# Kernel tuning notes

Measured on AMD Instinct MI355X. Metric: run time of the kernel, lower is better.

The kernel has to match this reference:

```python
import jax, jax.numpy as jnp
import numpy as np
from jax import lax

B, C, H, W = 8, 512, 64, 64
HM, WM = 256, 256
EPS = 1e-08


def _nearest_downsample(mask, H_out, W_out):
    # torch F.interpolate(mode='nearest'): src_idx = floor(dst_idx * in/out)
    h_in, w_in = mask.shape[-2:]
    ri = (jnp.arange(H_out) * h_in) // H_out
    ci = (jnp.arange(W_out) * w_in) // W_out
    return mask[:, :, ri][:, :, :, ci]


def _dilate3x3(m):
    # binary dilation with 3x3 ones structuring element == 3x3 max-pool, zero pad
    return lax.reduce_window(m, 0.0, lax.max, (1, 1, 3, 3), (1, 1, 1, 1),
                             [(0, 0), (0, 0), (1, 1), (1, 1)])


def _edt(mask2d):
    # Exact Euclidean distance from each pixel to nearest mask==1 pixel.
    # mask2d: [B, H, W] float 0/1. Separable two-pass squared EDT.
    b, h, w = mask2d.shape
    BIG = jnp.asarray(h + w, mask2d.dtype)
    rows = jnp.arange(h)
    di = jnp.abs(rows[:, None] - rows[None, :]).astype(mask2d.dtype)  # [H, H']
    # g[b,i,j] = min_{i'} |i - i'| s.t. mask[b,i',j]==1 (BIG if column empty)
    g = jnp.min(di[None, :, :, None] + BIG * (1.0 - mask2d)[:, None, :, :], axis=2)  # [B,H,W]
    cols = jnp.arange(w)
    dj2 = ((cols[:, None] - cols[None, :]) ** 2).astype(mask2d.dtype)  # [W, W']
    d2 = jnp.min(g[:, :, None, :] ** 2 + dj2[None, None, :, :], axis=3)  # [B,H,W]
    dist = jnp.sqrt(d2)
    dist = dist / (jnp.max(dist, axis=(1, 2), keepdims=True) + 1e-06)
    return dist


def setup_inputs() -> dict:
    key = jax.random.key(0)
    k1, k2, k3, k4, k5 = jax.random.split(key, 5)
    f_s = jax.random.normal(k1, (B, C, H, W), dtype=jnp.float32)
    support_mask = jax.random.randint(k2, (B, 1, HM, WM), 0, 2, dtype=jnp.int32)
    sg = 1.0 / np.sqrt(C)
    gate_w = jax.random.uniform(k3, (C, C), jnp.float32, -sg, sg)
    gate_b = jnp.zeros((C,), jnp.float32)
    sf = 1.0 / np.sqrt(C + 1)
    fusion_w = jax.random.uniform(k4, (C, C + 1), jnp.float32, -sf, sf)
    fusion_b = jnp.zeros((C,), jnp.float32)
    return {"f_s": f_s, "support_mask": support_mask, "gate_w": gate_w,
            "gate_b": gate_b, "fusion_w": fusion_w, "fusion_b": fusion_b}


def reference(f_s, support_mask, gate_w, gate_b, fusion_w, fusion_b):
    m_s = _nearest_downsample(support_mask, f_s.shape[2], f_s.shape[3]).astype(f_s.dtype)  # [B,1,H,W]
    m_dil = _dilate3x3(m_s)
    m_bg = jnp.clip(m_dil - m_s, 0.0, None)

    p_fg = jnp.sum(f_s * m_s, axis=(2, 3)) / (jnp.sum(m_s, axis=(2, 3)) + EPS)   # [B,C]
    p_bg = jnp.sum(f_s * m_bg, axis=(2, 3)) / (jnp.sum(m_bg, axis=(2, 3)) + EPS)  # [B,C]
    p_contrast = (p_fg - p_bg)[:, :, None, None]

    gate = jax.nn.sigmoid(jnp.einsum('bchw,oc->bohw', f_s, gate_w) + gate_b[None, :, None, None])
    f_pur = f_s + gate * p_contrast

    dist = _edt(m_s[:, 0])[:, None]  # [B,1,H,W]
    x = jnp.concatenate([f_pur, dist], axis=1)  # [B,C+1,H,W]
    out = jnp.einsum('bchw,oc->bohw', x, fusion_w) + fusion_b[None, :, None, None]
    return jax.nn.relu(out)
```

## Files before the change

kernel.cpp:

```cpp
#include <hip/hip_runtime.h>
#include <math.h>

#define NB 8
#define CC 512
#define NPIX 4096
#define HM 256

#define WS_MS    0
#define WS_MBG   32768
#define WS_DIST  65536
#define WS_CNT   98304
#define WS_PC    98320
#define WS_GWP   102416
#define WS_FWP   364560
#define WS_FSPK  626704
#define WS_FPPK  17403920

typedef __attribute__((ext_vector_type(8))) short short8;
typedef __attribute__((ext_vector_type(4))) float f32x4;

__device__ __forceinline__ uint32_t packbf(float x) {
    uint32_t b = __float_as_uint(x);
    uint32_t hi = (b + 0x7fffu + ((b >> 16) & 1u)) & 0xffff0000u;
    float rem = x - __uint_as_float(hi);
    uint32_t rb = __float_as_uint(rem);
    uint32_t lo = (rb + 0x7fffu + ((rb >> 16) & 1u)) >> 16;
    return hi | lo;
}
__device__ __forceinline__ float unpackf(uint32_t u) {
    return __uint_as_float(u & 0xffff0000u) + __uint_as_float(u << 16);
}

__device__ __forceinline__ float wave_sum(float v) {
#pragma unroll
    for (int o = 32; o > 0; o >>= 1) v += __shfl_down(v, o, 64);
    return v;
}
__device__ __forceinline__ float wave_max(float v) {
#pragma unroll
    for (int o = 32; o > 0; o >>= 1) v = fmaxf(v, __shfl_down(v, o, 64));
    return v;
}

__global__ __launch_bounds__(1024) void mask_edt_kernel(
    const int* __restrict__ mask, float* __restrict__ ms, float* __restrict__ mbg,
    float* __restrict__ dist, float* __restrict__ cnt)
{
    __shared__ float sm[4096];
    __shared__ float sg[4096];
    __shared__ float red[32];

    const int b = blockIdx.x;
    const int t = threadIdx.x;
    const int wid = t >> 6, lane = t & 63;
    const int* mb = mask + b * (HM * HM);

#pragma unroll
    for (int u = 0; u < 4; ++u) {
        int p = u * 1024 + t;
        int i = p >> 6, j = p & 63;
        sm[p] = (float)mb[(i * 4) * HM + (j * 4)];
    }
    __syncthreads();

    float cfg = 0.f, cbg = 0.f;
#pragma unroll
    for (int u = 0; u < 4; ++u) {
        int p = u * 1024 + t;
        int i = p >> 6, j = p & 63;
        float mx = 0.f;
#pragma unroll
        for (int di = -1; di <= 1; ++di) {
            int ii = i + di;
            if (ii < 0 || ii > 63) continue;
#pragma unroll
            for (int dj = -1; dj <= 1; ++dj) {
                int jj = j + dj;
                if (jj < 0 || jj > 63) continue;
                mx = fmaxf(mx, sm[ii * 64 + jj]);
            }
        }
        float m = sm[p];
        float bg = fmaxf(mx - m, 0.f);
        cfg += m; cbg += bg;
        ms[b * NPIX + p] = m;
        mbg[b * NPIX + p] = bg;
    }
    float s1 = wave_sum(cfg), s2 = wave_sum(cbg);
    if (lane == 0) { red[wid] = s1; red[16 + wid] = s2; }
    __syncthreads();
    if (t == 0) {
        float a = 0.f, g = 0.f;
#pragma unroll
        for (int w = 0; w < 16; ++w) { a += red[w]; g += red[16 + w]; }
        cnt[b] = a; cnt[8 + b] = g;
    }

#pragma unroll 1
    for (int u = 0; u < 4; ++u) {
        int p = u * 1024 + t;
        int i = p >> 6, j = p & 63;
        float fi = (float)i;
        float best = 1e30f;
#pragma unroll 8
        for (int ii = 0; ii < 64; ++ii) {
            float v = fabsf(fi - (float)ii) + 128.f * (1.f - sm[ii * 64 + j]);
            best = fminf(best, v);
        }
        sg[p] = best;
    }
    __syncthreads();

    float dmx = 0.f;
#pragma unroll 1
    for (int u = 0; u < 4; ++u) {
        int p = u * 1024 + t;
        int i = p >> 6, j = p & 63;
        float fj = (float)j;
        float best = 1e30f;
#pragma unroll 8
        for (int jj = 0; jj < 64; ++jj) {
            float g = sg[i * 64 + jj];
            float dj = fj - (float)jj;
            best = fminf(best, fmaf(g, g, dj * dj));
        }
        float d = sqrtf(best);
        sm[p] = d;
        dmx = fmaxf(dmx, d);
    }
    __syncthreads();
    float mW = wave_max(dmx);
    if (lane == 0) red[wid] = mW;
    __syncthreads();
    float dmax = red[0];
#pragma unroll
    for (int w = 1; w < 16; ++w) dmax = fmaxf(dmax, red[w]);
    dmax += 1e-6f;
#pragma unroll
    for (int u = 0; u < 4; ++u) {
        int p = u * 1024 + t;
        dist[b * NPIX + p] = sm[p] / dmax;
    }
}

__global__ __launch_bounds__(256) void pcontrast_kernel(
    const float* __restrict__ F, const float* __restrict__ ms,
    const float* __restrict__ mbg, const float* __restrict__ cnt,
    float* __restrict__ pc)
{
    const int c = blockIdx.x, b = blockIdx.y, t = threadIdx.x;
    const float4* f4 = (const float4*)(F + ((size_t)b * CC + c) * NPIX);
    const float4* m4 = (const float4*)(ms + (size_t)b * NPIX);
    const float4* g4 = (const float4*)(mbg + (size_t)b * NPIX);
    float sfg = 0.f, sbg = 0.f;
#pragma unroll 4
    for (int idx = t; idx < NPIX / 4; idx += 256) {
        float4 v = f4[idx], m = m4[idx], g = g4[idx];
        sfg += v.x * m.x + v.y * m.y + v.z * m.z + v.w * m.w;
        sbg += v.x * g.x + v.y * g.y + v.z * g.z + v.w * g.w;
    }
    __shared__ float r1[4], r2[4];
    sfg = wave_sum(sfg); sbg = wave_sum(sbg);
    int wid = t >> 6, lane = t & 63;
    if (lane == 0) { r1[wid] = sfg; r2[wid] = sbg; }
    __syncthreads();
    if (t == 0) {
        float a = r1[0] + r1[1] + r1[2] + r1[3];
        float g = r2[0] + r2[1] + r2[2] + r2[3];
        pc[b * CC + c] = a / (cnt[b] + 1e-8f) - g / (cnt[8 + b] + 1e-8f);
    }
}

__global__ __launch_bounds__(256) void transpose_pack(
    const float* __restrict__ F, uint32_t* __restrict__ Fp)
{
    __shared__ float sm[64][65];
    const int b  = blockIdx.z;
    const int c0 = blockIdx.y * 64;
    const int p0 = blockIdx.x * 64;
    const int t  = threadIdx.x;
    const float* Fb = F + ((size_t)b * CC + c0) * NPIX + p0;
#pragma unroll
    for (int s = 0; s < 4; ++s) {
        int cl = s * 16 + (t >> 4);
        float4 v = *(const float4*)&Fb[(size_t)cl * NPIX + (t & 15) * 4];
        *(float4*)&sm[cl][(t & 15) * 4] = v;
    }
    __syncthreads();
    const int lane = t & 63, w = t >> 6;
    uint32_t* Op = Fp + ((size_t)b * NPIX + p0) * CC + c0;
#pragma unroll
    for (int s = 0; s < 16; ++s) {
        int pl = s * 4 + w;
        Op[(size_t)pl * CC + lane] = packbf(sm[lane][pl]);
    }
}

__global__ __launch_bounds__(256) void pack_weights(
    const float* __restrict__ gw, const float* __restrict__ fw,
    uint32_t* __restrict__ gwp, uint32_t* __restrict__ fwp)
{
    const int o = blockIdx.x, t = threadIdx.x;
#pragma unroll 2
    for (int c = t; c < CC; c += 256) {
        gwp[o * CC + c] = packbf(gw[o * CC + c]);
        fwp[o * CC + c] = packbf(fw[o * (CC + 1) + c]);
    }
}

template <int MODE>
__global__ __launch_bounds__(256, 4) void mfma_gemm(
    const uint32_t* __restrict__ Apk, const uint32_t* __restrict__ Bpk,
    long aStride, long bStride,
    const float* __restrict__ bias,
    const float* __restrict__ aux,
    const float* __restrict__ wsrc,
    void* __restrict__ outp)
{
    const int gx = gridDim.x, gy = gridDim.y;
    const int nwg = gx * gy * gridDim.z;
    int lin = (blockIdx.z * gy + blockIdx.y) * gx + blockIdx.x;
    int cpx = nwg >> 3;
    int swz = (lin & 7) * cpx + (lin >> 3);
    const int bx = swz % gx;
    const int by = (swz / gx) % gy;
    const int b  = swz / (gx * gy);

    const int nBase = bx * 128;
    const int mBase = by * 128;
    const int tid   = threadIdx.x;
    const int lane  = tid & 63, wid = tid >> 6;
    const int wr    = wid >> 1, wc = wid & 1;

    __shared__ uint32_t As[128 * 32];
    __shared__ uint32_t Bs[128 * 32];

    const uint32_t* Ab = Apk + (size_t)b * aStride;
    const uint32_t* Bb = Bpk + (size_t)b * bStride;

    f32x4 acc[4][4];
#pragma unroll
    for (int i = 0; i < 4; ++i)
#pragma unroll
        for (int j = 0; j < 4; ++j) acc[i][j] = (f32x4){0.f, 0.f, 0.f, 0.f};

    const int l8 = lane >> 3;
    const int k16src = (lane & 7) ^ l8;
    const int fr = lane & 15;
    const int kc = lane >> 4;

    for (int it = 0; it < 16; ++it) {
        const int ktU = it * 32;
#pragma unroll
        for (int r = 0; r < 4; ++r) {
            int grp = r * 4 + wid;
            int row = grp * 8 + l8;
            const uint32_t* gA = Ab + (size_t)(mBase + row) * CC + ktU + k16src * 4;
            const uint32_t* gB = Bb + (size_t)(nBase + row) * CC + ktU + k16src * 4;
            __builtin_amdgcn_global_load_lds(
                (const __attribute__((address_space(1))) uint32_t*)gA,
                (__attribute__((address_space(3))) uint32_t*)&As[grp * 256 + lane * 4], 16, 0, 0);
            __builtin_amdgcn_global_load_lds(
                (const __attribute__((address_space(1))) uint32_t*)gB,
                (__attribute__((address_space(3))) uint32_t*)&Bs[grp * 256 + lane * 4], 16, 0, 0);
        }
        __syncthreads();

        short8 hA[4], lA[4];
#pragma unroll
        for (int fm = 0; fm < 4; ++fm) {
            int row = wr * 64 + fm * 16 + fr;
            int base = row * 32, s = row & 7;
            uint4 x0 = *(const uint4*)&As[base + (((kc * 2)     ^ s) << 2)];
            uint4 x1 = *(const uint4*)&As[base + (((kc * 2 + 1) ^ s) << 2)];
            uint32_t pk[8] = {x0.x, x0.y, x0.z, x0.w, x1.x, x1.y, x1.z, x1.w};
#pragma unroll
            for (int j = 0; j < 8; ++j) {
                hA[fm][j] = (short)(pk[j] >> 16);
                lA[fm][j] = (short)(pk[j] & 0xffffu);
            }
        }
#pragma unroll
        for (int fn = 0; fn < 4; ++fn) {
            int row = wc * 64 + fn * 16 + fr;
            int base = row * 32, s = row & 7;
            uint4 x0 = *(const uint4*)&Bs[base + (((kc * 2)     ^ s) << 2)];
            uint4 x1 = *(const uint4*)&Bs[base + (((kc * 2 + 1) ^ s) << 2)];
            uint32_t pk[8] = {x0.x, x0.y, x0.z, x0.w, x1.x, x1.y, x1.z, x1.w};
            short8 hB, lB;
#pragma unroll
            for (int j = 0; j < 8; ++j) {
                hB[j] = (short)(pk[j] >> 16);
                lB[j] = (short)(pk[j] & 0xffffu);
            }
#pragma unroll
            for (int fm = 0; fm < 4; ++fm) {
                acc[fm][fn] = __builtin_amdgcn_mfma_f32_16x16x32_bf16(hA[fm], hB, acc[fm][fn], 0, 0, 0);
                acc[fm][fn] = __builtin_amdgcn_mfma_f32_16x16x32_bf16(hA[fm], lB, acc[fm][fn], 0, 0, 0);
                acc[fm][fn] = __builtin_amdgcn_mfma_f32_16x16x32_bf16(lA[fm], hB, acc[fm][fn], 0, 0, 0);
            }
        }
        __syncthreads();
    }

    const int rrow = (lane >> 4) * 4;
    if constexpr (MODE == 0) {
        uint32_t* fpur = (uint32_t*)outp;
#pragma unroll
        for (int fn = 0; fn < 4; ++fn) {
            int o = nBase + wc * 64 + fn * 16 + fr;
            float bo  = bias[o];
            float pco = aux[(size_t)b * CC + o];
#pragma unroll
            for (int fm = 0; fm < 4; ++fm) {
#pragma unroll
                for (int r = 0; r < 4; ++r) {
                    int p = mBase + wr * 64 + fm * 16 + rrow + r;
                    size_t idx = (size_t)p * CC + o;
                    float fs = unpackf(Ab[idx]);
                    float z = acc[fm][fn][r] + bo;
                    float g = 1.f / (1.f + expf(-z));
                    fpur[(size_t)b * NPIX * CC + idx] = packbf(fs + g * pco);
                }
            }
        }
    } else {
        float* Out = (float*)outp;
#pragma unroll
        for (int fn = 0; fn < 4; ++fn) {
            int p = nBase + wc * 64 + fn * 16 + fr;
            float dv = aux[(size_t)b * NPIX + p];
#pragma unroll
            for (int fm = 0; fm < 4; ++fm) {
#pragma unroll
                for (int r = 0; r < 4; ++r) {
                    int o = mBase + wr * 64 + fm * 16 + rrow + r;
                    float z = acc[fm][fn][r] + bias[o] + wsrc[(size_t)o * (CC + 1) + CC] * dv;
                    Out[((size_t)b * CC + o) * NPIX + p] = fmaxf(z, 0.f);
                }
            }
        }
    }
}

extern "C" void kernel_launch(void* const* d_in, const int* in_sizes, int n_in,
                              void* d_out, int out_size, void* d_ws, size_t ws_size,
                              hipStream_t stream)
{
    const float* f_s      = (const float*)d_in[0];
    const int*   mask     = (const int*)d_in[1];
    const float* gate_w   = (const float*)d_in[2];
    const float* gate_b   = (const float*)d_in[3];
    const float* fusion_w = (const float*)d_in[4];
    const float* fusion_b = (const float*)d_in[5];
    float* out = (float*)d_out;
    float*    wsf = (float*)d_ws;
    uint32_t* wsu = (uint32_t*)d_ws;

    float* ms   = wsf + WS_MS;
    float* mbg  = wsf + WS_MBG;
    float* dist = wsf + WS_DIST;
    float* cnt  = wsf + WS_CNT;
    float* pc   = wsf + WS_PC;
    uint32_t* gwp  = wsu + WS_GWP;
    uint32_t* fwp  = wsu + WS_FWP;
    uint32_t* fspk = wsu + WS_FSPK;
    uint32_t* fppk = wsu + WS_FPPK;

    hipLaunchKernelGGL(mask_edt_kernel, dim3(NB), dim3(1024), 0, stream,
                       mask, ms, mbg, dist, cnt);
    hipLaunchKernelGGL(pack_weights, dim3(CC), dim3(256), 0, stream,
                       gate_w, fusion_w, gwp, fwp);
    hipLaunchKernelGGL(transpose_pack, dim3(NPIX / 64, CC / 64, NB), dim3(256), 0, stream,
                       f_s, fspk);
    hipLaunchKernelGGL(pcontrast_kernel, dim3(CC, NB), dim3(256), 0, stream,
                       f_s, ms, mbg, cnt, pc);
    hipLaunchKernelGGL((mfma_gemm<0>), dim3(CC / 128, NPIX / 128, NB), dim3(256), 0, stream,
                       fspk, gwp, (long)NPIX * CC, 0L, gate_b, pc, (const float*)nullptr,
                       (void*)fppk);
    hipLaunchKernelGGL((mfma_gemm<1>), dim3(NPIX / 128, CC / 128, NB), dim3(256), 0, stream,
                       fwp, fppk, 0L, (long)NPIX * CC, fusion_b, dist, fusion_w,
                       (void*)out);
}
```

Measured before the change: 405.0 us.

## Double-buffer LDS tiles in MFMA GEMM to overlap global loads with compute

Splits the shared-memory A/B tiles into two buffers and issues the async global-to-LDS loads for the next K tile before computing on the current one. This hides global load latency behind the MFMA work and halves the barrier count per tile pair. In exchange LDS use doubles to 64 KB per block and the occupancy hint in launch bounds drops from 4 to 2 blocks per CU, which may reduce latency hiding across waves.

```diff
diff --git a/kernel.cpp b/kernel.cpp
--- a/kernel.cpp
+++ b/kernel.cpp
@@ -208,8 +208,65 @@
     }
 }
 
+#define STAGE_TILE(dA, dB, ktU)                                                          \
+    do {                                                                                 \
+        _Pragma("unroll")                                                                \
+        for (int r_ = 0; r_ < 4; ++r_) {                                                 \
+            int grp_ = r_ * 4 + wid;                                                     \
+            int row_ = grp_ * 8 + l8;                                                    \
+            const uint32_t* gA_ = Ab + (size_t)(mBase + row_) * CC + (ktU) + k16src * 4; \
+            const uint32_t* gB_ = Bb + (size_t)(nBase + row_) * CC + (ktU) + k16src * 4; \
+            __builtin_amdgcn_global_load_lds(                                            \
+                (const __attribute__((address_space(1))) uint32_t*)gA_,                  \
+                (__attribute__((address_space(3))) uint32_t*)&dA[grp_ * 256 + lane * 4], \
+                16, 0, 0);                                                               \
+            __builtin_amdgcn_global_load_lds(                                            \
+                (const __attribute__((address_space(1))) uint32_t*)gB_,                  \
+                (__attribute__((address_space(3))) uint32_t*)&dB[grp_ * 256 + lane * 4], \
+                16, 0, 0);                                                               \
+        }                                                                                \
+    } while (0)
+
+#define COMPUTE_TILE(sA, sB)                                                             \
+    do {                                                                                 \
+        short8 hA_[4], lA_[4];                                                           \
+        _Pragma("unroll")                                                                \
+        for (int fm_ = 0; fm_ < 4; ++fm_) {                                              \
+            int row_ = wr * 64 + fm_ * 16 + fr;                                          \
+            int base_ = row_ * 32, s_ = row_ & 7;                                        \
+            uint4 x0_ = *(const uint4*)&sA[base_ + (((kc * 2)     ^ s_) << 2)];          \
+            uint4 x1_ = *(const uint4*)&sA[base_ + (((kc * 2 + 1) ^ s_) << 2)];          \
+            uint32_t pk_[8] = {x0_.x, x0_.y, x0_.z, x0_.w, x1_.x, x1_.y, x1_.z, x1_.w};  \
+            _Pragma("unroll")                                                            \
+            for (int j_ = 0; j_ < 8; ++j_) {                                             \
+                hA_[fm_][j_] = (short)(pk_[j_] >> 16);                                   \
+                lA_[fm_][j_] = (short)(pk_[j_] & 0xffffu);                               \
+            }                                                                            \
+        }                                                                                \
+        _Pragma("unroll")                                                                \
+        for (int fn_ = 0; fn_ < 4; ++fn_) {                                              \
+            int row_ = wc * 64 + fn_ * 16 + fr;                                          \
+            int base_ = row_ * 32, s_ = row_ & 7;                                        \
+            uint4 x0_ = *(const uint4*)&sB[base_ + (((kc * 2)     ^ s_) << 2)];          \
+            uint4 x1_ = *(const uint4*)&sB[base_ + (((kc * 2 + 1) ^ s_) << 2)];          \
+            uint32_t pk_[8] = {x0_.x, x0_.y, x0_.z, x0_.w, x1_.x, x1_.y, x1_.z, x1_.w};  \
+            short8 hB_, lB_;                                                             \
+            _Pragma("unroll")                                                            \
+            for (int j_ = 0; j_ < 8; ++j_) {                                             \
+                hB_[j_] = (short)(pk_[j_] >> 16);                                        \
+                lB_[j_] = (short)(pk_[j_] & 0xffffu);                                    \
+            }                                                                            \
+            _Pragma("unroll")                                                            \
+            for (int fm_ = 0; fm_ < 4; ++fm_) {                                          \
+                acc[fm_][fn_] = __builtin_amdgcn_mfma_f32_16x16x32_bf16(hA_[fm_], hB_, acc[fm_][fn_], 0, 0, 0); \
+                acc[fm_][fn_] = __builtin_amdgcn_mfma_f32_16x16x32_bf16(hA_[fm_], lB_, acc[fm_][fn_], 0, 0, 0); \
+                acc[fm_][fn_] = __builtin_amdgcn_mfma_f32_16x16x32_bf16(lA_[fm_], hB_, acc[fm_][fn_], 0, 0, 0); \
+            }                                                                            \
+        }                                                                                \
+    } while (0)
+
 template <int MODE>
-__global__ __launch_bounds__(256, 4) void mfma_gemm(
+__global__ __launch_bounds__(256, 2) void mfma_gemm(
     const uint32_t* __restrict__ Apk, const uint32_t* __restrict__ Bpk,
     long aStride, long bStride,
     const float* __restrict__ bias,
@@ -232,8 +289,10 @@
     const int lane  = tid & 63, wid = tid >> 6;
     const int wr    = wid >> 1, wc = wid & 1;
 
-    __shared__ uint32_t As[128 * 32];
-    __shared__ uint32_t Bs[128 * 32];
+    __shared__ uint32_t As0[128 * 32];
+    __shared__ uint32_t Bs0[128 * 32];
+    __shared__ uint32_t As1[128 * 32];
+    __shared__ uint32_t Bs1[128 * 32];
 
     const uint32_t* Ab = Apk + (size_t)b * aStride;
     const uint32_t* Bb = Bpk + (size_t)b * bStride;
@@ -249,57 +308,19 @@
     const int fr = lane & 15;
     const int kc = lane >> 4;
 
-    for (int it = 0; it < 16; ++it) {
-        const int ktU = it * 32;
-#pragma unroll
-        for (int r = 0; r < 4; ++r) {
-            int grp = r * 4 + wid;
-            int row = grp * 8 + l8;
-            const uint32_t* gA = Ab + (size_t)(mBase + row) * CC + ktU + k16src * 4;
-            const uint32_t* gB = Bb + (size_t)(nBase + row) * CC + ktU + k16src * 4;
-            __builtin_amdgcn_global_load_lds(
-                (const __attribute__((address_space(1))) uint32_t*)gA,
-                (__attribute__((address_space(3))) uint32_t*)&As[grp * 256 + lane * 4], 16, 0, 0);
-            __builtin_amdgcn_global_load_lds(
-                (const __attribute__((address_space(1))) uint32_t*)gB,
-                (__attribute__((address_space(3))) uint32_t*)&Bs[grp * 256 + lane * 4], 16, 0, 0);
-        }
+    STAGE_TILE(As0, Bs0, 0);
+    __syncthreads();
+
+#pragma unroll 1
+    for (int it2 = 0; it2 < 8; ++it2) {
+        const int ktU1 = it2 * 64 + 32;
+        STAGE_TILE(As1, Bs1, ktU1);
+        COMPUTE_TILE(As0, Bs0);
         __syncthreads();
-
-        short8 hA[4], lA[4];
-#pragma unroll
-        for (int fm = 0; fm < 4; ++fm) {
-            int row = wr * 64 + fm * 16 + fr;
-            int base = row * 32, s = row & 7;
-            uint4 x0 = *(const uint4*)&As[base + (((kc * 2)     ^ s) << 2)];
-            uint4 x1 = *(const uint4*)&As[base + (((kc * 2 + 1) ^ s) << 2)];
-            uint32_t pk[8] = {x0.x, x0.y, x0.z, x0.w, x1.x, x1.y, x1.z, x1.w};
-#pragma unroll
-            for (int j = 0; j < 8; ++j) {
-                hA[fm][j] = (short)(pk[j] >> 16);
-                lA[fm][j] = (short)(pk[j] & 0xffffu);
-            }
-        }
-#pragma unroll
-        for (int fn = 0; fn < 4; ++fn) {
-            int row = wc * 64 + fn * 16 + fr;
-            int base = row * 32, s = row & 7;
-            uint4 x0 = *(const uint4*)&Bs[base + (((kc * 2)     ^ s) << 2)];
-            uint4 x1 = *(const uint4*)&Bs[base + (((kc * 2 + 1) ^ s) << 2)];
-            uint32_t pk[8] = {x0.x, x0.y, x0.z, x0.w, x1.x, x1.y, x1.z, x1.w};
-            short8 hB, lB;
-#pragma unroll
-            for (int j = 0; j < 8; ++j) {
-                hB[j] = (short)(pk[j] >> 16);
-                lB[j] = (short)(pk[j] & 0xffffu);
-            }
-#pragma unroll
-            for (int fm = 0; fm < 4; ++fm) {
-                acc[fm][fn] = __builtin_amdgcn_mfma_f32_16x16x32_bf16(hA[fm], hB, acc[fm][fn], 0, 0, 0);
-                acc[fm][fn] = __builtin_amdgcn_mfma_f32_16x16x32_bf16(hA[fm], lB, acc[fm][fn], 0, 0, 0);
-                acc[fm][fn] = __builtin_amdgcn_mfma_f32_16x16x32_bf16(lA[fm], hB, acc[fm][fn], 0, 0, 0);
-            }
-        }
+        if (it2 < 7) {
+            STAGE_TILE(As0, Bs0, ktU1 + 32);
+        }
+        COMPUTE_TILE(As1, Bs1);
         __syncthreads();
     }
 
```

Result: faster. 344.5 us (-14.9%).
